# Kernel tuning notes

Measured on AMD Instinct MI355X. Metric: run time of the kernel, lower is better.

Reference implementation:

```python
import jax, jax.numpy as jnp
import numpy as np
from jax import lax

IMG_W, IMG_H = 800.0, 320.0
NPTS = 72
N_STRIPS = NPTS - 1
MAX_LANES = 4
NUM_PRIORS = 192
STAGES = 3
B = 512
LIOU_LEN = 15.0
CLS_W, XYT_W, IOU_W, SEG_W = 2.0, 0.2, 2.0, 1.0


def smooth_l1(x):
    ax = jnp.abs(x)
    return jnp.where(ax < 1.0, 0.5 * x * x, ax - 0.5)


def pairwise_line_iou(pred_xs, tgt_xs):
    # pred_xs [P,N] pixel xs, tgt_xs [L,N]; returns [P,L]
    px1, px2 = pred_xs - LIOU_LEN, pred_xs + LIOU_LEN
    tx1, tx2 = tgt_xs - LIOU_LEN, tgt_xs + LIOU_LEN
    ovr = jnp.minimum(px2[:, None, :], tx2[None]) - jnp.maximum(px1[:, None, :], tx1[None])
    union = jnp.maximum(px2[:, None, :], tx2[None]) - jnp.minimum(px1[:, None, :], tx1[None])
    invalid = (tgt_xs < 0) | (tgt_xs >= IMG_W)
    ovr = jnp.where(invalid[None], 0.0, ovr)
    union = jnp.where(invalid[None], 0.0, union)
    return ovr.sum(-1) / (union.sum(-1) + 1e-9)


def focal_sum(logits, target):
    # kornia-style softmax focal loss (alpha=0.25, gamma=2), summed
    p = jax.nn.softmax(logits, axis=1) + 1e-8
    focal = -0.25 * (1.0 - p) ** 2 * jnp.log(p)
    oh = jax.nn.one_hot(target, 2, dtype=logits.dtype)
    return (oh * focal).sum()


def per_sample(pred, tgt):
    # pred [P, 6+N], tgt [L, 6+N]
    L = tgt.shape[0]
    f32 = pred.dtype
    valid = tgt[:, 1] == 1.0
    num_t = valid.sum()
    has_t = num_t > 0

    t_xs = tgt[:, 6:]                          # [L,N] pixel xs (-1e5 = invalid)
    pred_xs_px = pred[:, 6:] * (IMG_W - 1.0)   # [P,N]
    iou_pair = pairwise_line_iou(pred_xs_px, t_xs)  # [P,L] (grad flows for loss)

    # ---------- assignment (stop-grad, mirrors CLRNet dynamic_assign) ----------
    pd = lax.stop_gradient(pred)
    pd_xs = pd[:, 6:] * (IMG_W - 1.0)
    inv_t = (t_xs < 0) | (t_xs >= IMG_W)
    t_len = (~inv_t).sum(1).astype(f32)
    dist = jnp.where(inv_t[None], 0.0, jnp.abs(t_xs[None] - pd_xs[:, None, :])).sum(-1)
    dist = dist / (t_len[None] + 1e-9)         # [P,L]

    def norm_score(x):
        m = jnp.max(jnp.where(valid[None], x, -jnp.inf))
        m = jnp.where(has_t, m, 1.0)
        return 1.0 - x / m + 1e-2

    dist_score = norm_score(dist)
    p_xy = jnp.stack([pd[:, 2] * (IMG_H - 1.0), pd[:, 3] * (IMG_W - 1.0)], 1)
    t_xy = jnp.stack([tgt[:, 2] * (IMG_H - 1.0), tgt[:, 3]], 1)
    sd = jnp.sqrt(((p_xy[:, None] - t_xy[None]) ** 2).sum(-1))
    s_score = norm_score(sd)
    th = jnp.abs(pd[:, 4, None] - tgt[None, :, 4]) * 180.0
    th_score = norm_score(th)
    sp = jax.nn.sigmoid(pd[:, :2])
    neg = -jnp.log(1.0 - sp + 1e-12) * 0.75 * sp ** 2
    pos = -jnp.log(sp + 1e-12) * 0.25 * (1.0 - sp) ** 2
    cls_cost = pos[:, 1] - neg[:, 1]           # all gt labels are 1
    cost = -(dist_score * s_score * th_score) ** 2 * 3.0 + cls_cost[:, None]
    cost = jnp.where(valid[None], cost, jnp.inf)

    # dynamic-k (SimOTA-style)
    iou_sg = jnp.where(valid[None], jnp.maximum(lax.stop_gradient(iou_pair), 0.0), 0.0)
    topk = lax.top_k(iou_sg.T, 4)[0]           # [L,4]
    dyn_k = jnp.maximum(topk.sum(1).astype(jnp.int32), 1)
    ranks = jnp.argsort(jnp.argsort(cost, axis=0), axis=0)
    M = (ranks < dyn_k[None]) & valid[None]
    multi = M.sum(1) > 1
    argmin_col = jnp.argmin(cost, axis=1)
    Mf = M.astype(f32)
    Mf = Mf.at[:, 0].set(jnp.where(multi, 0.0, Mf[:, 0]))
    oh_min = jax.nn.one_hot(argmin_col, L, dtype=f32)
    Mf = jnp.where(multi[:, None] & (oh_min > 0), 1.0, Mf)
    n_match = Mf.sum()

    # ---------- cls loss ----------
    cls_target = (Mf.sum(1) > 0).astype(jnp.int32)
    cls_term = focal_sum(pred[:, :2], cls_target) / jnp.where(has_t, num_t.astype(f32), 1.0)

    # ---------- reg yxtl (smooth L1) ----------
    scale = jnp.array([N_STRIPS, IMG_W - 1.0, 180.0, N_STRIPS], dtype=f32)
    pred_yxtl = pred[:, 2:6] * scale           # [P,4]
    tgt3 = jnp.stack([tgt[:, 2] * N_STRIPS, tgt[:, 3], tgt[:, 4] * 180.0], 1)  # [L,3]
    pred_starts = jnp.clip(jnp.round(lax.stop_gradient(pred[:, 2]) * N_STRIPS), 0, N_STRIPS)
    tgt_starts = jnp.round(tgt[:, 2] * N_STRIPS)
    tgt_len_pair = tgt[None, :, 5] - (pred_starts[:, None] - tgt_starts[None, :])  # [P,L]
    sl = smooth_l1(pred_yxtl[:, None, :3] - tgt3[None]).sum(-1) \
       + smooth_l1(pred_yxtl[:, 3][:, None] - tgt_len_pair)
    reg_term = (Mf * sl).sum() / jnp.maximum(n_match * 4.0, 1.0)
    iou_term = (Mf * (1.0 - iou_pair)).sum() / jnp.maximum(n_match, 1.0)
    zero = jnp.zeros((), f32)
    reg_term = jnp.where(has_t, reg_term, zero)
    iou_term = jnp.where(has_t, iou_term, zero)
    return cls_term, reg_term, iou_term


def setup_inputs() -> dict:
    key = jax.random.key(0)
    ks = jax.random.split(key, 8)
    D = 6 + NPTS
    cls = jax.random.normal(ks[0], (STAGES, B, NUM_PRIORS, 2), jnp.float32)
    rest = jax.random.uniform(ks[1], (STAGES, B, NUM_PRIORS, D - 2), dtype=jnp.float32)
    predictions = jnp.concatenate([cls, rest], -1)

    valid = jax.random.uniform(ks[2], (B, MAX_LANES)) < 0.8
    start = jax.random.randint(ks[3], (B, MAX_LANES), 0, 40)
    length = jax.random.randint(ks[4], (B, MAX_LANES), 10, NPTS)
    end = jnp.minimum(start + length, NPTS)
    idx = jnp.arange(NPTS)
    inside = (idx[None, None] >= start[..., None]) & (idx[None, None] < end[..., None]) & valid[..., None]
    xs = jax.random.uniform(ks[5], (B, MAX_LANES, NPTS), minval=0.0, maxval=IMG_W - 1.0)
    xs = jnp.where(inside, xs, -1e5)
    start_x = jnp.take_along_axis(xs, start[..., None], axis=-1)[..., 0]
    theta = jax.random.uniform(ks[6], (B, MAX_LANES), minval=0.3, maxval=0.9)
    vf = valid.astype(jnp.float32)
    neg = jnp.full((B, MAX_LANES), -1e5, jnp.float32)
    targets = jnp.full((B, MAX_LANES, D), -1e5, jnp.float32)
    targets = targets.at[..., 0].set(1.0 - vf)
    targets = targets.at[..., 1].set(vf)
    targets = targets.at[..., 2].set(jnp.where(valid, start.astype(jnp.float32) / N_STRIPS, neg))
    targets = targets.at[..., 3].set(jnp.where(valid, start_x, neg))
    targets = targets.at[..., 4].set(jnp.where(valid, theta, neg))
    targets = targets.at[..., 5].set(jnp.where(valid, (end - start).astype(jnp.float32), neg))
    targets = targets.at[..., 6:].set(xs)

    seg_loss = jax.random.uniform(ks[7], (), dtype=jnp.float32)
    return {"predictions": predictions, "targets": targets, "seg_loss": seg_loss}


def reference(predictions, targets, seg_loss):
    per_batch = jax.vmap(per_sample)
    cls_l = jnp.zeros((), predictions.dtype)
    reg_l = jnp.zeros((), predictions.dtype)
    iou_l = jnp.zeros((), predictions.dtype)
    for s in range(predictions.shape[0]):  # 3 refine stages (fixed)
        c, r, i = per_batch(predictions[s], targets)
        cls_l = cls_l + c.sum()
        reg_l = reg_l + r.sum()
        iou_l = iou_l + i.sum()
    denom = targets.shape[0] * predictions.shape[0]
    cls_l = cls_l / denom
    reg_l = reg_l / denom
    iou_l = iou_l / denom
    return cls_l * CLS_W + reg_l * XYT_W + iou_l * IOU_W + seg_loss * SEG_W
```

## Files before the change

kernel.cpp:

```cpp
#include <hip/hip_runtime.h>
#include <math.h>

constexpr int kNpts   = 72;
constexpr int kPriors = 192;
constexpr int kLanes  = 4;
constexpr int kBatch  = 512;
constexpr int kStages = 3;
constexpr int kD      = 6 + kNpts;

typedef unsigned long long u64;

__device__ __forceinline__ float smoothL1(float x) {
  float ax = fabsf(x);
  return ax < 1.0f ? 0.5f * x * x : ax - 0.5f;
}

__device__ __forceinline__ unsigned ordF(float f) {
  unsigned b = __float_as_uint(f);
  return (b & 0x80000000u) ? ~b : (b | 0x80000000u);
}

__device__ __forceinline__ void cswapA(u64& a, u64& b) {
  if (b < a) { u64 t = a; a = b; b = t; }
}
__device__ __forceinline__ void cswapD(float& a, float& b) {
  if (b > a) { float t = a; a = b; b = t; }
}

__global__ void clr_init(const float* __restrict__ seg, float* __restrict__ out) {
  out[0] = seg[0];
}

__global__ __launch_bounds__(192) void clr_loss_kernel(
    const float* __restrict__ pred,
    const float* __restrict__ tgt,
    float* __restrict__ out) {
  const int blk  = blockIdx.x;
  const int b    = blk & (kBatch - 1);
  const int tid  = threadIdx.x;
  const int wav  = tid >> 6;
  const int lane = tid & 63;

  __shared__ float s_tx[kNpts][kLanes];
  __shared__ float s_m [kNpts][kLanes];
  __shared__ float s_hdr[kLanes][6];
  __shared__ float s_cost[kLanes][kPriors];
  __shared__ float s_iou[kLanes][kPriors];
  __shared__ u64   s_thr[kLanes];
  __shared__ float s_sc[3][4];

  const float* tg = tgt + (size_t)b * kLanes * kD;
  for (int t = tid; t < kLanes * kNpts; t += 192) {
    int j = t / kNpts, k = t - j * kNpts;
    float v = tg[j * kD + 6 + k];
    s_tx[k][j] = v;
    s_m [k][j] = (v >= 0.0f && v < 800.0f) ? 1.0f : 0.0f;
  }
  if (tid < kLanes * 6) {
    int j = tid / 6, c = tid - j * 6;
    s_hdr[j][c] = tg[j * kD + c];
  }

  const float*  pr   = pred + ((size_t)blk * kPriors + tid) * kD;
  const float2* rowv = (const float2*)pr;
  float2 h0 = rowv[0], h1 = rowv[1], h2 = rowv[2];
  float px[kNpts];
#pragma unroll
  for (int q = 0; q < 36; ++q) {
    float2 v = rowv[3 + q];
    px[2 * q]     = v.x * 799.0f;
    px[2 * q + 1] = v.y * 799.0f;
  }
  const float p0 = h0.x, p1 = h0.y, p2 = h1.x, p3 = h1.y, p4 = h2.x, p5 = h2.y;

  __syncthreads();

  bool validL[kLanes];
  int num_t = 0;
#pragma unroll
  for (int j = 0; j < kLanes; ++j) {
    validL[j] = (s_hdr[j][1] == 1.0f);
    num_t += validL[j] ? 1 : 0;
  }
  const bool has_t = num_t > 0;

  float ds[kLanes] = {0.0f, 0.0f, 0.0f, 0.0f};
  {
    const float4* tx4 = (const float4*)&s_tx[0][0];
    const float4* m4  = (const float4*)&s_m[0][0];
#pragma unroll
    for (int k = 0; k < kNpts; ++k) {
      float4 t = tx4[k];
      float4 m = m4[k];
      float p = px[k];
      ds[0] = fmaf(m.x, fabsf(t.x - p), ds[0]);
      ds[1] = fmaf(m.y, fabsf(t.y - p), ds[1]);
      ds[2] = fmaf(m.z, fabsf(t.z - p), ds[2]);
      ds[3] = fmaf(m.w, fabsf(t.w - p), ds[3]);
    }
  }

  float iou[kLanes], dist[kLanes], sd[kLanes], th[kLanes];
  float md = -INFINITY, ms = -INFINITY, mt = -INFINITY;
  const float py = p2 * 319.0f, pxc = p3 * 799.0f;
#pragma unroll
  for (int j = 0; j < kLanes; ++j) {
    float tlen = validL[j] ? s_hdr[j][5] : 0.0f;
    float ovr = fmaf(tlen, 30.0f, -ds[j]);
    float uni = fmaf(tlen, 30.0f,  ds[j]) + 1e-9f;
    iou[j]  = ovr / uni;
    dist[j] = ds[j] / (tlen + 1e-9f);
    float dy = py - s_hdr[j][2] * 319.0f;
    float dx = pxc - s_hdr[j][3];
    sd[j] = sqrtf(dy * dy + dx * dx);
    th[j] = fabsf(p4 - s_hdr[j][4]) * 180.0f;
    if (validL[j]) {
      md = fmaxf(md, dist[j]);
      ms = fmaxf(ms, sd[j]);
      mt = fmaxf(mt, th[j]);
    }
  }

#pragma unroll
  for (int off = 32; off; off >>= 1) {
    md = fmaxf(md, __shfl_down(md, off, 64));
    ms = fmaxf(ms, __shfl_down(ms, off, 64));
    mt = fmaxf(mt, __shfl_down(mt, off, 64));
  }
  if (lane == 0) { s_sc[wav][0] = md; s_sc[wav][1] = ms; s_sc[wav][2] = mt; }
  __syncthreads();
  md = fmaxf(fmaxf(s_sc[0][0], s_sc[1][0]), s_sc[2][0]);
  ms = fmaxf(fmaxf(s_sc[0][1], s_sc[1][1]), s_sc[2][1]);
  mt = fmaxf(fmaxf(s_sc[0][2], s_sc[1][2]), s_sc[2][2]);
  if (!has_t) { md = 1.0f; ms = 1.0f; mt = 1.0f; }

  const float sp1  = 1.0f / (1.0f + expf(-p1));
  const float neg1 = -logf(1.0f - sp1 + 1e-12f) * 0.75f * sp1 * sp1;
  const float om1  = 1.0f - sp1;
  const float pos1 = -logf(sp1 + 1e-12f) * 0.25f * om1 * om1;
  const float cls_cost = pos1 - neg1;

  float costr[kLanes];
#pragma unroll
  for (int j = 0; j < kLanes; ++j) {
    s_iou[j][tid] = validL[j] ? fmaxf(iou[j], 0.0f) : 0.0f;
    float c;
    if (validL[j]) {
      float a = (1.0f - dist[j] / md) + 0.01f;
      float s = (1.0f - sd[j] / ms) + 0.01f;
      float t = (1.0f - th[j] / mt) + 0.01f;
      float g = a * s * t;
      c = cls_cost - g * g * 3.0f;
    } else {
      c = INFINITY;
    }
    costr[j] = c;
    s_cost[j][tid] = c;
  }
  __syncthreads();

  for (int j = wav; j < kLanes; j += 3) {
    u64 k0, k1, k2, k3;
    {
      float c0 = s_cost[j][lane], c1 = s_cost[j][lane + 64], c2 = s_cost[j][lane + 128];
      k0 = ((u64)ordF(c0) << 32) | (unsigned)lane;
      k1 = ((u64)ordF(c1) << 32) | (unsigned)(lane + 64);
      k2 = ((u64)ordF(c2) << 32) | (unsigned)(lane + 128);
      k3 = 0xFFFFFFFFFFFFFFFFull;
      cswapA(k0, k1); cswapA(k0, k2); cswapA(k1, k2);
#pragma unroll
      for (int off = 1; off < 64; off <<= 1) {
        u64 b0 = __shfl_xor(k0, off), b1 = __shfl_xor(k1, off);
        u64 b2 = __shfl_xor(k2, off), b3 = __shfl_xor(k3, off);
        u64 m0 = k0 < b3 ? k0 : b3, m1 = k1 < b2 ? k1 : b2;
        u64 m2 = k2 < b1 ? k2 : b1, m3 = k3 < b0 ? k3 : b0;
        cswapA(m0, m2); cswapA(m1, m3); cswapA(m0, m1); cswapA(m2, m3);
        k0 = m0; k1 = m1; k2 = m2; k3 = m3;
      }
    }
    float t0, t1, t2, t3;
    {
      t0 = s_iou[j][lane]; t1 = s_iou[j][lane + 64]; t2 = s_iou[j][lane + 128];
      t3 = -1.0f;
      cswapD(t0, t1); cswapD(t0, t2); cswapD(t1, t2);
#pragma unroll
      for (int off = 1; off < 64; off <<= 1) {
        float b0 = __shfl_xor(t0, off), b1 = __shfl_xor(t1, off);
        float b2 = __shfl_xor(t2, off), b3 = __shfl_xor(t3, off);
        float m0 = fmaxf(t0, b3), m1 = fmaxf(t1, b2);
        float m2 = fmaxf(t2, b1), m3 = fmaxf(t3, b0);
        cswapD(m0, m2); cswapD(m1, m3); cswapD(m0, m1); cswapD(m2, m3);
        t0 = m0; t1 = m1; t2 = m2; t3 = m3;
      }
    }
    if (lane == 0) {
      float s = ((t0 + t1) + t2) + t3;
      int dk = (int)s;
      if (dk < 1) dk = 1;
      if (dk > 4) dk = 4;
      s_thr[j] = dk == 1 ? k0 : dk == 2 ? k1 : dk == 3 ? k2 : k3;
    }
  }
  __syncthreads();

  int Mi[kLanes];
  int msum = 0;
#pragma unroll
  for (int j = 0; j < kLanes; ++j) {
    u64 myk = ((u64)ordF(costr[j]) << 32) | (unsigned)tid;
    Mi[j] = (validL[j] && myk <= s_thr[j]) ? 1 : 0;
    msum += Mi[j];
  }

  float amin = costr[0];
  int aidx = 0;
#pragma unroll
  for (int j = 1; j < kLanes; ++j)
    if (costr[j] < amin) { amin = costr[j]; aidx = j; }

  float Mf[kLanes];
#pragma unroll
  for (int j = 0; j < kLanes; ++j) Mf[j] = (float)Mi[j];
  if (msum > 1) {
    Mf[0] = 0.0f;
    Mf[aidx] = 1.0f;
  }

  const float mfsum = Mf[0] + Mf[1] + Mf[2] + Mf[3];
  const int cls_t = (mfsum > 0.0f) ? 1 : 0;

  const float mx = fmaxf(p0, p1);
  const float e0 = expf(p0 - mx), e1 = expf(p1 - mx);
  const float inv = 1.0f / (e0 + e1);
  const float q = (cls_t ? e1 : e0) * inv + 1e-8f;
  const float omq = 1.0f - q;
  const float focal = -0.25f * omq * omq * logf(q);

  const float pred_start = fminf(fmaxf(rintf(p2 * 71.0f), 0.0f), 71.0f);
  const float py0 = p2 * 71.0f, py1 = p3 * 799.0f, py2t = p4 * 180.0f, py3 = p5 * 71.0f;
  float regc = 0.0f, iouc = 0.0f;
#pragma unroll
  for (int j = 0; j < kLanes; ++j) {
    if (Mf[j] > 0.0f) {
      float t30 = s_hdr[j][2] * 71.0f;
      float t31 = s_hdr[j][3];
      float t32 = s_hdr[j][4] * 180.0f;
      float tstart = rintf(s_hdr[j][2] * 71.0f);
      float tlp = s_hdr[j][5] - (pred_start - tstart);
      regc += smoothL1(py0 - t30) + smoothL1(py1 - t31) + smoothL1(py2t - t32)
            + smoothL1(py3 - tlp);
      iouc += 1.0f - iou[j];
    }
  }

  float v0 = mfsum, v1 = focal, v2 = regc, v3 = iouc;
#pragma unroll
  for (int off = 32; off; off >>= 1) {
    v0 += __shfl_down(v0, off, 64);
    v1 += __shfl_down(v1, off, 64);
    v2 += __shfl_down(v2, off, 64);
    v3 += __shfl_down(v3, off, 64);
  }
  __syncthreads();
  if (lane == 0) {
    s_sc[wav][0] = v0; s_sc[wav][1] = v1; s_sc[wav][2] = v2; s_sc[wav][3] = v3;
  }
  __syncthreads();

  if (tid == 0) {
    float nm      = s_sc[0][0] + s_sc[1][0] + s_sc[2][0];
    float cls_sum = s_sc[0][1] + s_sc[1][1] + s_sc[2][1];
    float reg_sum = s_sc[0][2] + s_sc[1][2] + s_sc[2][2];
    float iou_sum = s_sc[0][3] + s_sc[1][3] + s_sc[2][3];

    float cls_term = cls_sum / (has_t ? (float)num_t : 1.0f);
    float reg_term = has_t ? reg_sum / fmaxf(nm * 4.0f, 1.0f) : 0.0f;
    float iou_term = has_t ? iou_sum / fmaxf(nm, 1.0f) : 0.0f;

    float sample = 2.0f * cls_term + 0.2f * reg_term + 2.0f * iou_term;
    atomicAdd(out, sample * (1.0f / (float)(kBatch * kStages)));
  }
}

extern "C" void kernel_launch(void* const* d_in, const int* in_sizes, int n_in,
                              void* d_out, int out_size, void* d_ws, size_t ws_size,
                              hipStream_t stream) {
  const float* pred = (const float*)d_in[0];
  const float* tgt  = (const float*)d_in[1];
  const float* seg  = (const float*)d_in[2];
  float* out = (float*)d_out;

  clr_init<<<1, 1, 0, stream>>>(seg, out);
  clr_loss_kernel<<<kStages * kBatch, 192, 0, stream>>>(pred, tgt, out);
}
```

Measured before the change: 148.7 us.

## Stage prediction rows via coalesced double-buffered LDS and trim top-k to three

Prediction rows are now copied into shared memory in 64-row chunks with coalesced float4 loads, double-buffered so the next chunk loads while one wave computes distances from the current chunk. This replaces the strided per-thread row loads. The dynamic-k selection now keeps only the top three cost keys with a cheaper merge network. The cost sort and the IoU sort run as separate wave tasks, and invalid lanes are skipped. The trade-offs are serialized distance compute across waves, about 40KB of LDS per block that can lower occupancy, and a dk clamp at 3 instead of 4 that could diverge from the reference in rare cases.

```diff
diff --git a/kernel.cpp b/kernel.cpp
--- a/kernel.cpp
+++ b/kernel.cpp
@@ -7,6 +7,9 @@
 constexpr int kBatch  = 512;
 constexpr int kStages = 3;
 constexpr int kD      = 6 + kNpts;
+constexpr int kChunkRows = 64;
+constexpr int kChunkF = kChunkRows * kD;
+constexpr int kChunkV4 = kChunkF / 4;
 
 typedef unsigned long long u64;
 
@@ -26,6 +29,8 @@
 __device__ __forceinline__ void cswapD(float& a, float& b) {
   if (b > a) { float t = a; a = b; b = t; }
 }
+__device__ __forceinline__ u64 umin64(u64 a, u64 b) { return a < b ? a : b; }
+__device__ __forceinline__ u64 umax64(u64 a, u64 b) { return a < b ? b : a; }
 
 __global__ void clr_init(const float* __restrict__ seg, float* __restrict__ out) {
   out[0] = seg[0];
@@ -41,13 +46,18 @@
   const int wav  = tid >> 6;
   const int lane = tid & 63;
 
+  __shared__ alignas(16) float s_buf[2][kChunkF];
   __shared__ float s_tx[kNpts][kLanes];
   __shared__ float s_m [kNpts][kLanes];
   __shared__ float s_hdr[kLanes][6];
   __shared__ float s_cost[kLanes][kPriors];
   __shared__ float s_iou[kLanes][kPriors];
-  __shared__ u64   s_thr[kLanes];
+  __shared__ u64   s_k3[kLanes][3];
+  __shared__ int   s_dk[kLanes];
   __shared__ float s_sc[3][4];
+
+  const float*  gsrc = pred + (size_t)blk * (kPriors * kD);
+  const float4* g4   = (const float4*)gsrc;
 
   const float* tg = tgt + (size_t)b * kLanes * kD;
   for (int t = tid; t < kLanes * kNpts; t += 192) {
@@ -60,19 +70,16 @@
     int j = tid / 6, c = tid - j * 6;
     s_hdr[j][c] = tg[j * kD + c];
   }
-
-  const float*  pr   = pred + ((size_t)blk * kPriors + tid) * kD;
-  const float2* rowv = (const float2*)pr;
-  float2 h0 = rowv[0], h1 = rowv[1], h2 = rowv[2];
-  float px[kNpts];
-#pragma unroll
-  for (int q = 0; q < 36; ++q) {
-    float2 v = rowv[3 + q];
-    px[2 * q]     = v.x * 799.0f;
-    px[2 * q + 1] = v.y * 799.0f;
-  }
-  const float p0 = h0.x, p1 = h0.y, p2 = h1.x, p3 = h1.y, p4 = h2.x, p5 = h2.y;
-
+  if (tid < kLanes) {
+    s_dk[tid] = 1; s_k3[tid][0] = 0; s_k3[tid][1] = 0; s_k3[tid][2] = 0;
+  }
+
+  {
+    float4* d4 = (float4*)&s_buf[0][0];
+#pragma unroll
+    for (int it = 0; it < 6; ++it) d4[it * 192 + tid] = g4[it * 192 + tid];
+    if (tid < kChunkV4 - 6 * 192) d4[1152 + tid] = g4[1152 + tid];
+  }
   __syncthreads();
 
   bool validL[kLanes];
@@ -84,36 +91,56 @@
   }
   const bool has_t = num_t > 0;
 
-  float ds[kLanes] = {0.0f, 0.0f, 0.0f, 0.0f};
-  {
-    const float4* tx4 = (const float4*)&s_tx[0][0];
-    const float4* m4  = (const float4*)&s_m[0][0];
-#pragma unroll
-    for (int k = 0; k < kNpts; ++k) {
-      float4 t = tx4[k];
-      float4 m = m4[k];
-      float p = px[k];
-      ds[0] = fmaf(m.x, fabsf(t.x - p), ds[0]);
-      ds[1] = fmaf(m.y, fabsf(t.y - p), ds[1]);
-      ds[2] = fmaf(m.z, fabsf(t.z - p), ds[2]);
-      ds[3] = fmaf(m.w, fabsf(t.w - p), ds[3]);
-    }
-  }
+  float p0 = 0, p1 = 0, p2v = 0, p3v = 0, p4v = 0, p5v = 0;
+  float ds0 = 0, ds1 = 0, ds2 = 0, ds3 = 0;
+  for (int p = 0; p < 3; ++p) {
+    if (p < 2) {
+      float4* d4 = (float4*)&s_buf[(p + 1) & 1][0];
+      const float4* s4 = g4 + (p + 1) * kChunkV4;
+#pragma unroll
+      for (int it = 0; it < 6; ++it) d4[it * 192 + tid] = s4[it * 192 + tid];
+      if (tid < kChunkV4 - 6 * 192) d4[1152 + tid] = s4[1152 + tid];
+    }
+    if (wav == p) {
+      const float2* L2 = (const float2*)(&s_buf[p & 1][0] + lane * kD);
+      float2 h0 = L2[0], h1 = L2[1], h2 = L2[2];
+      p0 = h0.x; p1 = h0.y; p2v = h1.x; p3v = h1.y; p4v = h2.x; p5v = h2.y;
+      const float4* tx4 = (const float4*)&s_tx[0][0];
+      const float4* m4  = (const float4*)&s_m[0][0];
+#pragma unroll
+      for (int i = 0; i < 36; ++i) {
+        float2 a = L2[3 + i];
+        float pA = a.x * 799.0f, pB = a.y * 799.0f;
+        float4 tA = tx4[2 * i],     mA = m4[2 * i];
+        float4 tB = tx4[2 * i + 1], mB = m4[2 * i + 1];
+        ds0 = fmaf(mA.x, fabsf(tA.x - pA), ds0);
+        ds1 = fmaf(mA.y, fabsf(tA.y - pA), ds1);
+        ds2 = fmaf(mA.z, fabsf(tA.z - pA), ds2);
+        ds3 = fmaf(mA.w, fabsf(tA.w - pA), ds3);
+        ds0 = fmaf(mB.x, fabsf(tB.x - pB), ds0);
+        ds1 = fmaf(mB.y, fabsf(tB.y - pB), ds1);
+        ds2 = fmaf(mB.z, fabsf(tB.z - pB), ds2);
+        ds3 = fmaf(mB.w, fabsf(tB.w - pB), ds3);
+      }
+    }
+    __syncthreads();
+  }
+  float dsA[kLanes] = {ds0, ds1, ds2, ds3};
 
   float iou[kLanes], dist[kLanes], sd[kLanes], th[kLanes];
   float md = -INFINITY, ms = -INFINITY, mt = -INFINITY;
-  const float py = p2 * 319.0f, pxc = p3 * 799.0f;
+  const float py = p2v * 319.0f, pxc = p3v * 799.0f;
 #pragma unroll
   for (int j = 0; j < kLanes; ++j) {
     float tlen = validL[j] ? s_hdr[j][5] : 0.0f;
-    float ovr = fmaf(tlen, 30.0f, -ds[j]);
-    float uni = fmaf(tlen, 30.0f,  ds[j]) + 1e-9f;
+    float ovr = fmaf(tlen, 30.0f, -dsA[j]);
+    float uni = fmaf(tlen, 30.0f,  dsA[j]) + 1e-9f;
     iou[j]  = ovr / uni;
-    dist[j] = ds[j] / (tlen + 1e-9f);
+    dist[j] = dsA[j] / (tlen + 1e-9f);
     float dy = py - s_hdr[j][2] * 319.0f;
     float dx = pxc - s_hdr[j][3];
     sd[j] = sqrtf(dy * dy + dx * dx);
-    th[j] = fabsf(p4 - s_hdr[j][4]) * 180.0f;
+    th[j] = fabsf(p4v - s_hdr[j][4]) * 180.0f;
     if (validL[j]) {
       md = fmaxf(md, dist[j]);
       ms = fmaxf(ms, sd[j]);
@@ -159,29 +186,29 @@
   }
   __syncthreads();
 
-  for (int j = wav; j < kLanes; j += 3) {
-    u64 k0, k1, k2, k3;
-    {
+  for (int t = wav; t < 8; t += 3) {
+    const int j = t & 3;
+    if (!validL[j]) continue;
+    if (t < 4) {
       float c0 = s_cost[j][lane], c1 = s_cost[j][lane + 64], c2 = s_cost[j][lane + 128];
-      k0 = ((u64)ordF(c0) << 32) | (unsigned)lane;
-      k1 = ((u64)ordF(c1) << 32) | (unsigned)(lane + 64);
-      k2 = ((u64)ordF(c2) << 32) | (unsigned)(lane + 128);
-      k3 = 0xFFFFFFFFFFFFFFFFull;
+      u64 k0 = ((u64)ordF(c0) << 32) | (unsigned)lane;
+      u64 k1 = ((u64)ordF(c1) << 32) | (unsigned)(lane + 64);
+      u64 k2 = ((u64)ordF(c2) << 32) | (unsigned)(lane + 128);
       cswapA(k0, k1); cswapA(k0, k2); cswapA(k1, k2);
 #pragma unroll
       for (int off = 1; off < 64; off <<= 1) {
-        u64 b0 = __shfl_xor(k0, off), b1 = __shfl_xor(k1, off);
-        u64 b2 = __shfl_xor(k2, off), b3 = __shfl_xor(k3, off);
-        u64 m0 = k0 < b3 ? k0 : b3, m1 = k1 < b2 ? k1 : b2;
-        u64 m2 = k2 < b1 ? k2 : b1, m3 = k3 < b0 ? k3 : b0;
-        cswapA(m0, m2); cswapA(m1, m3); cswapA(m0, m1); cswapA(m2, m3);
-        k0 = m0; k1 = m1; k2 = m2; k3 = m3;
+        u64 b0 = __shfl_xor(k0, off), b1 = __shfl_xor(k1, off), b2 = __shfl_xor(k2, off);
+        u64 x0 = umin64(k0, b0), y0 = umax64(k0, b0);
+        u64 x1 = umin64(k1, b1);
+        u64 mc = umin64(k2, b2);
+        k0 = x0;
+        k2 = umin64(umax64(y0, x1), mc);
+        k1 = umin64(y0, x1);
       }
-    }
-    float t0, t1, t2, t3;
-    {
-      t0 = s_iou[j][lane]; t1 = s_iou[j][lane + 64]; t2 = s_iou[j][lane + 128];
-      t3 = -1.0f;
+      if (lane == 0) { s_k3[j][0] = k0; s_k3[j][1] = k1; s_k3[j][2] = k2; }
+    } else {
+      float t0 = s_iou[j][lane], t1 = s_iou[j][lane + 64], t2 = s_iou[j][lane + 128];
+      float t3 = -1.0f;
       cswapD(t0, t1); cswapD(t0, t2); cswapD(t1, t2);
 #pragma unroll
       for (int off = 1; off < 64; off <<= 1) {
@@ -192,13 +219,13 @@
         cswapD(m0, m2); cswapD(m1, m3); cswapD(m0, m1); cswapD(m2, m3);
         t0 = m0; t1 = m1; t2 = m2; t3 = m3;
       }
-    }
-    if (lane == 0) {
-      float s = ((t0 + t1) + t2) + t3;
-      int dk = (int)s;
-      if (dk < 1) dk = 1;
-      if (dk > 4) dk = 4;
-      s_thr[j] = dk == 1 ? k0 : dk == 2 ? k1 : dk == 3 ? k2 : k3;
+      if (lane == 0) {
+        float s = ((t0 + t1) + t2) + t3;
+        int dk = (int)s;
+        if (dk < 1) dk = 1;
+        if (dk > 3) dk = 3;
+        s_dk[j] = dk;
+      }
     }
   }
   __syncthreads();
@@ -208,7 +235,7 @@
 #pragma unroll
   for (int j = 0; j < kLanes; ++j) {
     u64 myk = ((u64)ordF(costr[j]) << 32) | (unsigned)tid;
-    Mi[j] = (validL[j] && myk <= s_thr[j]) ? 1 : 0;
+    Mi[j] = (validL[j] && myk <= s_k3[j][s_dk[j] - 1]) ? 1 : 0;
     msum += Mi[j];
   }
 
@@ -236,8 +263,8 @@
   const float omq = 1.0f - q;
   const float focal = -0.25f * omq * omq * logf(q);
 
-  const float pred_start = fminf(fmaxf(rintf(p2 * 71.0f), 0.0f), 71.0f);
-  const float py0 = p2 * 71.0f, py1 = p3 * 799.0f, py2t = p4 * 180.0f, py3 = p5 * 71.0f;
+  const float pred_start = fminf(fmaxf(rintf(p2v * 71.0f), 0.0f), 71.0f);
+  const float py0 = p2v * 71.0f, py1 = p3v * 799.0f, py2t = p4v * 180.0f, py3 = p5v * 71.0f;
   float regc = 0.0f, iouc = 0.0f;
 #pragma unroll
   for (int j = 0; j < kLanes; ++j) {
```

Measured after the change: 165.5 us. 11.3% more time.

## Split top-k and IoU sort across waves, replace atomics with partial-sum reduce kernel

Applied to the files above, without the earlier changes.

The per-lane assignment work is split into eight independent tasks, a cost top-3 sort and an IoU top-4 sort per lane, spread over the three waves. Lanes without a target are skipped. The cost sort keeps only three keys, merged with a cheaper min/max network, and dynamic k is clamped to 3. The global atomicAdd is replaced by a per-block partial written to workspace plus a single reduce kernel that also adds seg_loss, removing the init kernel. Clamping k to 3 changes behaviour if the summed IoU could reach 4, and the extra launch adds a little fixed cost.

```diff
diff --git a/kernel.cpp b/kernel.cpp
--- a/kernel.cpp
+++ b/kernel.cpp
@@ -7,6 +7,7 @@
 constexpr int kBatch  = 512;
 constexpr int kStages = 3;
 constexpr int kD      = 6 + kNpts;
+constexpr int kBlocks = kStages * kBatch;
 
 typedef unsigned long long u64;
 
@@ -26,15 +27,13 @@
 __device__ __forceinline__ void cswapD(float& a, float& b) {
   if (b > a) { float t = a; a = b; b = t; }
 }
-
-__global__ void clr_init(const float* __restrict__ seg, float* __restrict__ out) {
-  out[0] = seg[0];
-}
+__device__ __forceinline__ u64 umin64(u64 a, u64 b) { return a < b ? a : b; }
+__device__ __forceinline__ u64 umax64(u64 a, u64 b) { return a < b ? b : a; }
 
 __global__ __launch_bounds__(192) void clr_loss_kernel(
     const float* __restrict__ pred,
     const float* __restrict__ tgt,
-    float* __restrict__ out) {
+    float* __restrict__ partial) {
   const int blk  = blockIdx.x;
   const int b    = blk & (kBatch - 1);
   const int tid  = threadIdx.x;
@@ -46,7 +45,8 @@
   __shared__ float s_hdr[kLanes][6];
   __shared__ float s_cost[kLanes][kPriors];
   __shared__ float s_iou[kLanes][kPriors];
-  __shared__ u64   s_thr[kLanes];
+  __shared__ u64   s_k3[kLanes][3];
+  __shared__ int   s_dk[kLanes];
   __shared__ float s_sc[3][4];
 
   const float* tg = tgt + (size_t)b * kLanes * kD;
@@ -59,6 +59,10 @@
   if (tid < kLanes * 6) {
     int j = tid / 6, c = tid - j * 6;
     s_hdr[j][c] = tg[j * kD + c];
+  }
+  if (tid >= 64 && tid < 64 + kLanes) {
+    int j = tid - 64;
+    s_dk[j] = 1; s_k3[j][0] = 0; s_k3[j][1] = 0; s_k3[j][2] = 0;
   }
 
   const float*  pr   = pred + ((size_t)blk * kPriors + tid) * kD;
@@ -159,29 +163,29 @@
   }
   __syncthreads();
 
-  for (int j = wav; j < kLanes; j += 3) {
-    u64 k0, k1, k2, k3;
-    {
+  for (int t = wav; t < 8; t += 3) {
+    const int j = t & 3;
+    if (!validL[j]) continue;
+    if (t < 4) {
       float c0 = s_cost[j][lane], c1 = s_cost[j][lane + 64], c2 = s_cost[j][lane + 128];
-      k0 = ((u64)ordF(c0) << 32) | (unsigned)lane;
-      k1 = ((u64)ordF(c1) << 32) | (unsigned)(lane + 64);
-      k2 = ((u64)ordF(c2) << 32) | (unsigned)(lane + 128);
-      k3 = 0xFFFFFFFFFFFFFFFFull;
+      u64 k0 = ((u64)ordF(c0) << 32) | (unsigned)lane;
+      u64 k1 = ((u64)ordF(c1) << 32) | (unsigned)(lane + 64);
+      u64 k2 = ((u64)ordF(c2) << 32) | (unsigned)(lane + 128);
       cswapA(k0, k1); cswapA(k0, k2); cswapA(k1, k2);
 #pragma unroll
       for (int off = 1; off < 64; off <<= 1) {
-        u64 b0 = __shfl_xor(k0, off), b1 = __shfl_xor(k1, off);
-        u64 b2 = __shfl_xor(k2, off), b3 = __shfl_xor(k3, off);
-        u64 m0 = k0 < b3 ? k0 : b3, m1 = k1 < b2 ? k1 : b2;
-        u64 m2 = k2 < b1 ? k2 : b1, m3 = k3 < b0 ? k3 : b0;
-        cswapA(m0, m2); cswapA(m1, m3); cswapA(m0, m1); cswapA(m2, m3);
-        k0 = m0; k1 = m1; k2 = m2; k3 = m3;
+        u64 b0 = __shfl_xor(k0, off), b1 = __shfl_xor(k1, off), b2 = __shfl_xor(k2, off);
+        u64 x0 = umin64(k0, b0), y0 = umax64(k0, b0);
+        u64 x1 = umin64(k1, b1);
+        u64 mc = umin64(k2, b2);
+        k0 = x0;
+        k2 = umin64(umax64(y0, x1), mc);
+        k1 = umin64(y0, x1);
       }
-    }
-    float t0, t1, t2, t3;
-    {
-      t0 = s_iou[j][lane]; t1 = s_iou[j][lane + 64]; t2 = s_iou[j][lane + 128];
-      t3 = -1.0f;
+      if (lane == 0) { s_k3[j][0] = k0; s_k3[j][1] = k1; s_k3[j][2] = k2; }
+    } else {
+      float t0 = s_iou[j][lane], t1 = s_iou[j][lane + 64], t2 = s_iou[j][lane + 128];
+      float t3 = -1.0f;
       cswapD(t0, t1); cswapD(t0, t2); cswapD(t1, t2);
 #pragma unroll
       for (int off = 1; off < 64; off <<= 1) {
@@ -192,13 +196,13 @@
         cswapD(m0, m2); cswapD(m1, m3); cswapD(m0, m1); cswapD(m2, m3);
         t0 = m0; t1 = m1; t2 = m2; t3 = m3;
       }
-    }
-    if (lane == 0) {
-      float s = ((t0 + t1) + t2) + t3;
-      int dk = (int)s;
-      if (dk < 1) dk = 1;
-      if (dk > 4) dk = 4;
-      s_thr[j] = dk == 1 ? k0 : dk == 2 ? k1 : dk == 3 ? k2 : k3;
+      if (lane == 0) {
+        float s = ((t0 + t1) + t2) + t3;
+        int dk = (int)s;
+        if (dk < 1) dk = 1;
+        if (dk > 3) dk = 3;
+        s_dk[j] = dk;
+      }
     }
   }
   __syncthreads();
@@ -208,7 +212,7 @@
 #pragma unroll
   for (int j = 0; j < kLanes; ++j) {
     u64 myk = ((u64)ordF(costr[j]) << 32) | (unsigned)tid;
-    Mi[j] = (validL[j] && myk <= s_thr[j]) ? 1 : 0;
+    Mi[j] = (validL[j] && myk <= s_k3[j][s_dk[j] - 1]) ? 1 : 0;
     msum += Mi[j];
   }
 
@@ -277,8 +281,29 @@
     float reg_term = has_t ? reg_sum / fmaxf(nm * 4.0f, 1.0f) : 0.0f;
     float iou_term = has_t ? iou_sum / fmaxf(nm, 1.0f) : 0.0f;
 
-    float sample = 2.0f * cls_term + 0.2f * reg_term + 2.0f * iou_term;
-    atomicAdd(out, sample * (1.0f / (float)(kBatch * kStages)));
+    partial[blk] = 2.0f * cls_term + 0.2f * reg_term + 2.0f * iou_term;
+  }
+}
+
+__global__ __launch_bounds__(256) void clr_reduce(
+    const float* __restrict__ partial,
+    const float* __restrict__ seg,
+    float* __restrict__ out) {
+  const int tid  = threadIdx.x;
+  const int wav  = tid >> 6;
+  const int lane = tid & 63;
+  __shared__ float sc[4];
+
+  float s = 0.0f;
+#pragma unroll
+  for (int i = 0; i < kBlocks / 256; ++i) s += partial[tid + 256 * i];
+#pragma unroll
+  for (int off = 32; off; off >>= 1) s += __shfl_down(s, off, 64);
+  if (lane == 0) sc[wav] = s;
+  __syncthreads();
+  if (tid == 0) {
+    float tot = ((sc[0] + sc[1]) + sc[2]) + sc[3];
+    out[0] = tot * (1.0f / (float)kBlocks) + seg[0];
   }
 }
 
@@ -288,8 +313,9 @@
   const float* pred = (const float*)d_in[0];
   const float* tgt  = (const float*)d_in[1];
   const float* seg  = (const float*)d_in[2];
-  float* out = (float*)d_out;
-
-  clr_init<<<1, 1, 0, stream>>>(seg, out);
-  clr_loss_kernel<<<kStages * kBatch, 192, 0, stream>>>(pred, tgt, out);
-}
+  float* out     = (float*)d_out;
+  float* partial = (float*)d_ws;
+
+  clr_loss_kernel<<<kBlocks, 192, 0, stream>>>(pred, tgt, partial);
+  clr_reduce<<<1, 256, 0, stream>>>(partial, seg, out);
+}
```

After: 146.4 us. No clear change (-1.6%).
